# Kernel tuning notes

Hardware: AMD Instinct MI355X
Metric: run time of the kernel (lower is better)

Reference implementation:

```python
import jax, jax.numpy as jnp
import numpy as np

DIM, H, HD = 512, 8, 64
N_BANK = 4096
EPS = 1e-5


def layernorm(x, g, b):
    m = jnp.mean(x, axis=-1, keepdims=True)
    v = jnp.mean(jnp.square(x - m), axis=-1, keepdims=True)
    return (x - m) * jax.lax.rsqrt(v + EPS) * g + b


def setup_inputs() -> dict:
    key = jax.random.key(0)
    ks = jax.random.split(key, 8)
    # xavier_uniform bound for square (512,512) linears
    bound = float(np.sqrt(6.0 / (DIM + DIM)))
    inp = {
        "x_q": jax.random.normal(ks[0], (32, 128, DIM), jnp.float32),
        "x_k": jax.random.normal(ks[1], (N_BANK, DIM), jnp.float32),
        "x_v": jax.random.normal(ks[2], (N_BANK, DIM), jnp.float32),
        "Wq": jax.random.uniform(ks[3], (DIM, DIM), jnp.float32, -bound, bound),
        "Wk": jax.random.uniform(ks[4], (DIM, DIM), jnp.float32, -bound, bound),
        "Wv": jax.random.uniform(ks[5], (DIM, DIM), jnp.float32, -bound, bound),
        "Wproj": jax.random.uniform(ks[6], (DIM, DIM), jnp.float32, -bound, bound),
        "qn_g": jnp.ones((HD,), jnp.float32),
        "qn_b": jnp.zeros((HD,), jnp.float32),
        "kn_g": jnp.ones((HD,), jnp.float32),
        "kn_b": jnp.zeros((HD,), jnp.float32),
        "n_g": jnp.ones((DIM,), jnp.float32),
        "n_b": jnp.zeros((DIM,), jnp.float32),
    }
    return inp


def reference(x_q, x_k, x_v, Wq, Wk, Wv, Wproj, qn_g, qn_b, kn_g, kn_b, n_g, n_b):
    B, S, D = x_q.shape
    N = x_k.shape[0]
    scale = HD ** (-0.5)
    # Linear layers (torch: y = x @ W.T)
    q = jnp.einsum('bsd,od->bso', x_q, Wq).reshape(B, S, H, HD).transpose(0, 2, 1, 3)  # (B,H,S,hd)
    k = jnp.einsum('nd,od->no', x_k, Wk).reshape(N, H, HD).transpose(1, 0, 2)          # (H,N,hd)
    v = jnp.einsum('nd,od->no', x_v, Wv).reshape(N, H, HD).transpose(1, 0, 2)          # (H,N,hd)
    # per-head qk layernorm
    q = layernorm(q, qn_g, qn_b) * scale
    k = layernorm(k, kn_g, kn_b)
    # cross-attention to shared bank (K/V have no batch dim)
    attn = jnp.einsum('bhsd,hnd->bhsn', q, k)          # (B,H,S,N)
    attn = jax.nn.softmax(attn, axis=-1)
    x = jnp.einsum('bhsn,hnd->bhsd', attn, v)          # (B,H,S,hd)
    x = x.transpose(0, 2, 1, 3).reshape(B, S, D)
    x = layernorm(x, n_g, n_b)
    x = jnp.einsum('bsd,od->bso', x, Wproj)
    return x
```

## Files before the change

kernel.cpp:

```cpp
#include <hip/hip_runtime.h>
#include <hip/hip_bf16.h>
#include <math.h>

#define DIM 512
#define NHEAD 8
#define HD 64
#define NBANK 4096
#define NQROWS 4096
#define EPS 1e-5f
#define QSCALE 0.125f
#define PART_ELEMS (NQROWS * DIM)

typedef __attribute__((ext_vector_type(4))) float floatx4;
typedef __attribute__((ext_vector_type(8))) short short8;

__device__ __forceinline__ unsigned short f2bf(float f) {
    unsigned int u = __float_as_uint(f);
    u += 0x7fffu + ((u >> 16) & 1u);
    return (unsigned short)(u >> 16);
}
__device__ __forceinline__ float bf2f(unsigned short h) {
    return __uint_as_float(((unsigned int)h) << 16);
}
__device__ __forceinline__ unsigned int pk2(float a, float b) {
    union { __hip_bfloat162 h; unsigned int u; } cvt;
    cvt.h = __float22bfloat162_rn(make_float2(a, b));
    return cvt.u;
}

__global__ __launch_bounds__(256) void wcvt_kernel(
    const float* __restrict__ Wq, const float* __restrict__ Wk,
    const float* __restrict__ Wv, const float* __restrict__ Wp,
    unsigned short* __restrict__ Wb)
{
    const float* src = (blockIdx.y == 0) ? Wq : (blockIdx.y == 1) ? Wk
                     : (blockIdx.y == 2) ? Wv : Wp;
    unsigned short* dst = Wb + (size_t)blockIdx.y * DIM * DIM;
    const int i = (blockIdx.x * 256 + threadIdx.x) * 8;
    const float4 a0 = *(const float4*)(src + i);
    const float4 a1 = *(const float4*)(src + i + 4);
    union { short8 v; unsigned int u[4]; } t;
    t.u[0] = pk2(a0.x, a0.y); t.u[1] = pk2(a0.z, a0.w);
    t.u[2] = pk2(a1.x, a1.y); t.u[3] = pk2(a1.z, a1.w);
    *(short8*)(dst + i) = t.v;
}

__global__ __launch_bounds__(256) void qkv_kernel(
    const float* __restrict__ xq, const float* __restrict__ xk, const float* __restrict__ xv,
    const unsigned short* __restrict__ Wb,
    const float* __restrict__ qg, const float* __restrict__ qbeta,
    const float* __restrict__ kg, const float* __restrict__ kbeta,
    unsigned short* __restrict__ Qb, unsigned short* __restrict__ Kb,
    unsigned short* __restrict__ VTb)
{
    __shared__ short8 smem[3072];
    const int tid  = threadIdx.x;
    const int w    = tid >> 6, lane = tid & 63, m = lane & 15, q = lane >> 4;
    const int wr   = w & 1, wc = w >> 1;
    const int row0 = blockIdx.x * 64;
    const int mat  = blockIdx.y >> 2;
    const int col0 = (blockIdx.y & 3) * 128;
    const float* X = (mat == 0) ? xq : (mat == 1) ? xk : xv;
    const unsigned short* Wm = Wb + (size_t)mat * DIM * DIM;

    const int arow0 = tid >> 3,           aseg = tid & 7;
    const int arow1 = (tid + 256) >> 3;
    const float* ap0 = X + (size_t)(row0 + arow0) * DIM + aseg * 8;
    const float* ap1 = X + (size_t)(row0 + arow1) * DIM + aseg * 8;
    const int adst0 = arow0 * 8 + (aseg ^ (arow0 & 7));
    const int adst1 = arow1 * 8 + (aseg ^ (arow1 & 7));
    int brow[4], bdst[4];
    const unsigned short* bp[4];
    #pragma unroll
    for (int j = 0; j < 4; ++j) {
        const int idx = tid + j * 256;
        brow[j] = idx >> 3; const int seg = idx & 7;
        bp[j] = Wm + (size_t)(col0 + brow[j]) * DIM + seg * 8;
        bdst[j] = brow[j] * 8 + (seg ^ (brow[j] & 7));
    }

    floatx4 acc[2][4];
    #pragma unroll
    for (int mt = 0; mt < 2; ++mt)
        #pragma unroll
        for (int nt = 0; nt < 4; ++nt) acc[mt][nt] = (floatx4){0.f, 0.f, 0.f, 0.f};

    float4 pa[4];
    short8 pb[4];

    pa[0] = *(const float4*)(ap0);     pa[1] = *(const float4*)(ap0 + 4);
    pa[2] = *(const float4*)(ap1);     pa[3] = *(const float4*)(ap1 + 4);
    #pragma unroll
    for (int j = 0; j < 4; ++j) pb[j] = *(const short8*)(bp[j]);
    {
        short8* as = smem; short8* bs = smem + 512;
        union { short8 v; unsigned int u[4]; } ta;
        ta.u[0] = pk2(pa[0].x, pa[0].y); ta.u[1] = pk2(pa[0].z, pa[0].w);
        ta.u[2] = pk2(pa[1].x, pa[1].y); ta.u[3] = pk2(pa[1].z, pa[1].w);
        as[adst0] = ta.v;
        ta.u[0] = pk2(pa[2].x, pa[2].y); ta.u[1] = pk2(pa[2].z, pa[2].w);
        ta.u[2] = pk2(pa[3].x, pa[3].y); ta.u[3] = pk2(pa[3].z, pa[3].w);
        as[adst1] = ta.v;
        #pragma unroll
        for (int j = 0; j < 4; ++j) bs[bdst[j]] = pb[j];
    }
    pa[0] = *(const float4*)(ap0 + 64);  pa[1] = *(const float4*)(ap0 + 68);
    pa[2] = *(const float4*)(ap1 + 64);  pa[3] = *(const float4*)(ap1 + 68);
    #pragma unroll
    for (int j = 0; j < 4; ++j) pb[j] = *(const short8*)(bp[j] + 64);
    __syncthreads();

    for (int kt = 0; kt < 8; ++kt) {
        short8* as  = smem + (kt & 1) * 1536;
        short8* bs  = as + 512;
        short8* asn = smem + ((kt + 1) & 1) * 1536;
        short8* bsn = asn + 512;
        if (kt < 7) {
            union { short8 v; unsigned int u[4]; } ta;
            ta.u[0] = pk2(pa[0].x, pa[0].y); ta.u[1] = pk2(pa[0].z, pa[0].w);
            ta.u[2] = pk2(pa[1].x, pa[1].y); ta.u[3] = pk2(pa[1].z, pa[1].w);
            asn[adst0] = ta.v;
            ta.u[0] = pk2(pa[2].x, pa[2].y); ta.u[1] = pk2(pa[2].z, pa[2].w);
            ta.u[2] = pk2(pa[3].x, pa[3].y); ta.u[3] = pk2(pa[3].z, pa[3].w);
            asn[adst1] = ta.v;
            #pragma unroll
            for (int j = 0; j < 4; ++j) bsn[bdst[j]] = pb[j];
        }
        if (kt < 6) {
            const int o = (kt + 2) * 64;
            pa[0] = *(const float4*)(ap0 + o);  pa[1] = *(const float4*)(ap0 + o + 4);
            pa[2] = *(const float4*)(ap1 + o);  pa[3] = *(const float4*)(ap1 + o + 4);
            #pragma unroll
            for (int j = 0; j < 4; ++j) pb[j] = *(const short8*)(bp[j] + o);
        }
        #pragma unroll
        for (int s = 0; s < 2; ++s) {
            short8 af[2], bfr[4];
            #pragma unroll
            for (int mt = 0; mt < 2; ++mt)
                af[mt] = as[(wr * 32 + mt * 16 + m) * 8 + ((s * 4 + q) ^ (m & 7))];
            #pragma unroll
            for (int nt = 0; nt < 4; ++nt)
                bfr[nt] = bs[(wc * 64 + nt * 16 + m) * 8 + ((s * 4 + q) ^ (m & 7))];
            #pragma unroll
            for (int mt = 0; mt < 2; ++mt)
                #pragma unroll
                for (int nt = 0; nt < 4; ++nt)
                    acc[mt][nt] = __builtin_amdgcn_mfma_f32_16x16x32_bf16(af[mt], bfr[nt], acc[mt][nt], 0, 0, 0);
        }
        __syncthreads();
    }

    if (mat < 2) {
        const float* g = (mat == 0) ? qg : kg;
        const float* be = (mat == 0) ? qbeta : kbeta;
        unsigned short* Y = (mat == 0) ? Qb : Kb;
        float gv[4], bv[4];
        #pragma unroll
        for (int nt = 0; nt < 4; ++nt) { gv[nt] = g[nt * 16 + m]; bv[nt] = be[nt * 16 + m]; }
        #pragma unroll
        for (int mt = 0; mt < 2; ++mt) {
            #pragma unroll
            for (int r = 0; r < 4; ++r) {
                float s = 0.f, sq = 0.f;
                #pragma unroll
                for (int nt = 0; nt < 4; ++nt) { const float v = acc[mt][nt][r]; s += v; sq += v * v; }
                s  += __shfl_xor(s, 1);  s  += __shfl_xor(s, 2);  s  += __shfl_xor(s, 4);  s  += __shfl_xor(s, 8);
                sq += __shfl_xor(sq, 1); sq += __shfl_xor(sq, 2); sq += __shfl_xor(sq, 4); sq += __shfl_xor(sq, 8);
                const float mean = s * (1.f / HD);
                const float var  = sq * (1.f / HD) - mean * mean;
                const float rr   = rsqrtf(var + EPS);
                const int grow = row0 + wr * 32 + mt * 16 + q * 4 + r;
                #pragma unroll
                for (int nt = 0; nt < 4; ++nt) {
                    float v = (acc[mt][nt][r] - mean) * rr * gv[nt] + bv[nt];
                    if (mat == 0) v *= QSCALE;
                    Y[(size_t)grow * DIM + col0 + wc * 64 + nt * 16 + m] = f2bf(v);
                }
            }
        }
    } else {
        unsigned short* vt = (unsigned short*)smem;
        #pragma unroll
        for (int mt = 0; mt < 2; ++mt)
            #pragma unroll
            for (int nt = 0; nt < 4; ++nt) {
                const int c  = wc * 64 + nt * 16 + m;
                const int rw = wr * 32 + mt * 16 + q * 4;
                *(unsigned int*)(vt + c * 88 + rw)     = pk2(acc[mt][nt][0], acc[mt][nt][1]);
                *(unsigned int*)(vt + c * 88 + rw + 2) = pk2(acc[mt][nt][2], acc[mt][nt][3]);
            }
        __syncthreads();
        #pragma unroll
        for (int p = 0; p < 4; ++p) {
            const int idx = tid + p * 256;
            const int c = idx >> 3, sg = idx & 7;
            *(short8*)(VTb + (size_t)(col0 + c) * NBANK + row0 + sg * 8) =
                *(const short8*)(vt + c * 88 + sg * 8);
        }
    }
}

__global__ __launch_bounds__(256) void attn_kernel(
    const unsigned short* __restrict__ Qb, const unsigned short* __restrict__ Kb,
    const unsigned short* __restrict__ VTb, unsigned short* __restrict__ AOp,
    float* __restrict__ sums)
{
    __shared__ short8 smem[2048];
    const int tid  = threadIdx.x;
    const int w    = tid >> 6;
    const int lane = tid & 63;
    const int m    = lane & 15;
    const int Qd   = lane >> 4;
    const int h    = blockIdx.x & 7;
    const int qgi  = blockIdx.x >> 3;
    const int row0 = qgi * 128;
    const int part = blockIdx.y;
    const int base0 = part * 1024;

    const int sn0 = tid >> 3,        sseg = tid & 7;
    const int sn1 = (tid + 256) >> 3;
    const int kd0 = sn0 * 8 + (sseg ^ (sn0 & 7));
    const int kd1 = sn1 * 8 + (sseg ^ (sn1 & 7));
    const unsigned short* kp0 = Kb + (size_t)sn0 * DIM + h * HD + sseg * 8;
    const unsigned short* kp1 = Kb + (size_t)sn1 * DIM + h * HD + sseg * 8;
    const unsigned short* vp0 = VTb + (size_t)(h * HD + sn0) * NBANK + (sseg >> 2) * 32 + (sseg & 3) * 4;
    const unsigned short* vp1 = VTb + (size_t)(h * HD + sn1) * NBANK + (sseg >> 2) * 32 + (sseg & 3) * 4;

    short8 qf[2][2];
    #pragma unroll
    for (int mt = 0; mt < 2; ++mt)
        #pragma unroll
        for (int s = 0; s < 2; ++s)
            qf[mt][s] = *(const short8*)(Qb + (size_t)(row0 + w * 32 + mt * 16 + m) * DIM
                                         + h * HD + s * 32 + Qd * 8);

    floatx4 of[4][2];
    float sump[2] = {0.f, 0.f};
    #pragma unroll
    for (int t = 0; t < 4; ++t)
        #pragma unroll
        for (int mt = 0; mt < 2; ++mt) of[t][mt] = (floatx4){0.f, 0.f, 0.f, 0.f};

    short8 kreg0, kreg1;
    ushort4 vlo0, vhi0, vlo1, vhi1;

    kreg0 = *(const short8*)(kp0 + (size_t)base0 * DIM);
    kreg1 = *(const short8*)(kp1 + (size_t)base0 * DIM);
    vlo0 = *(const ushort4*)(vp0 + base0);  vhi0 = *(const ushort4*)(vp0 + base0 + 16);
    vlo1 = *(const ushort4*)(vp1 + base0);  vhi1 = *(const ushort4*)(vp1 + base0 + 16);
    {
        short8* ks = smem; short8* vts = smem + 512;
        ks[kd0] = kreg0; ks[kd1] = kreg1;
        union { short8 v; ushort4 h4[2]; } tv;
        tv.h4[0] = vlo0; tv.h4[1] = vhi0;  vts[kd0] = tv.v;
        tv.h4[0] = vlo1; tv.h4[1] = vhi1;  vts[kd1] = tv.v;
    }
    kreg0 = *(const short8*)(kp0 + (size_t)(base0 + 64) * DIM);
    kreg1 = *(const short8*)(kp1 + (size_t)(base0 + 64) * DIM);
    vlo0 = *(const ushort4*)(vp0 + base0 + 64);  vhi0 = *(const ushort4*)(vp0 + base0 + 80);
    vlo1 = *(const ushort4*)(vp1 + base0 + 64);  vhi1 = *(const ushort4*)(vp1 + base0 + 80);
    __syncthreads();

    for (int c = 0; c < 16; ++c) {
        short8* ks   = smem + (c & 1) * 1024;
        short8* vts  = ks + 512;
        short8* ksn  = smem + ((c + 1) & 1) * 1024;
        short8* vtsn = ksn + 512;
        if (c < 15) {
            ksn[kd0] = kreg0; ksn[kd1] = kreg1;
            union { short8 v; ushort4 h4[2]; } tv;
            tv.h4[0] = vlo0; tv.h4[1] = vhi0;  vtsn[kd0] = tv.v;
            tv.h4[0] = vlo1; tv.h4[1] = vhi1;  vtsn[kd1] = tv.v;
        }
        if (c < 14) {
            const int nb = base0 + (c + 2) * 64;
            kreg0 = *(const short8*)(kp0 + (size_t)nb * DIM);
            kreg1 = *(const short8*)(kp1 + (size_t)nb * DIM);
            vlo0 = *(const ushort4*)(vp0 + nb);  vhi0 = *(const ushort4*)(vp0 + nb + 16);
            vlo1 = *(const ushort4*)(vp1 + nb);  vhi1 = *(const ushort4*)(vp1 + nb + 16);
        }

        floatx4 st[4][2];
        #pragma unroll
        for (int t = 0; t < 4; ++t)
            #pragma unroll
            for (int mt = 0; mt < 2; ++mt) st[t][mt] = (floatx4){0.f, 0.f, 0.f, 0.f};
        #pragma unroll
        for (int s = 0; s < 2; ++s)
            #pragma unroll
            for (int t = 0; t < 4; ++t) {
                const short8 kf = ks[(t * 16 + m) * 8 + ((s * 4 + Qd) ^ (m & 7))];
                #pragma unroll
                for (int mt = 0; mt < 2; ++mt)
                    st[t][mt] = __builtin_amdgcn_mfma_f32_16x16x32_bf16(kf, qf[mt][s], st[t][mt], 0, 0, 0);
            }

        float p[4][2][4];
        #pragma unroll
        for (int t = 0; t < 4; ++t)
            #pragma unroll
            for (int mt = 0; mt < 2; ++mt)
                #pragma unroll
                for (int r = 0; r < 4; ++r) {
                    const float e = __expf(st[t][mt][r]);
                    p[t][mt][r] = e;
                    sump[mt] += e;
                }
        union { short8 v; unsigned int u[4]; } pf[2][2];
        #pragma unroll
        for (int mt = 0; mt < 2; ++mt)
            #pragma unroll
            for (int s2 = 0; s2 < 2; ++s2)
                #pragma unroll
                for (int u = 0; u < 4; ++u)
                    pf[mt][s2].u[u] = pk2(p[s2 * 2 + (u >> 1)][mt][(u & 1) * 2],
                                          p[s2 * 2 + (u >> 1)][mt][(u & 1) * 2 + 1]);

        #pragma unroll
        for (int s2 = 0; s2 < 2; ++s2)
            #pragma unroll
            for (int t2 = 0; t2 < 4; ++t2) {
                const short8 vf = vts[(t2 * 16 + m) * 8 + ((s2 * 4 + Qd) ^ (m & 7))];
                #pragma unroll
                for (int mt = 0; mt < 2; ++mt)
                    of[t2][mt] = __builtin_amdgcn_mfma_f32_16x16x32_bf16(vf, pf[mt][s2].v, of[t2][mt], 0, 0, 0);
            }
        __syncthreads();
    }

    #pragma unroll
    for (int mt = 0; mt < 2; ++mt) {
        float s = sump[mt];
        s += __shfl_xor(s, 16);
        s += __shfl_xor(s, 32);
        sump[mt] = s;
    }
    if (Qd == 0) {
        #pragma unroll
        for (int mt = 0; mt < 2; ++mt)
            sums[((size_t)part * NQROWS + row0 + w * 32 + mt * 16 + m) * NHEAD + h] = sump[mt];
    }

    unsigned int* ob = (unsigned int*)smem;
    #pragma unroll
    for (int t2 = 0; t2 < 4; ++t2)
        #pragma unroll
        for (int mt = 0; mt < 2; ++mt) {
            const int q  = w * 32 + mt * 16 + m;
            const int blk = t2 * 2 + (Qd >> 1);
            const int sub = (Qd & 1) * 2;
            const int bs  = (blk ^ (q & 7)) * 4;
            ob[q * 32 + bs + sub]     = pk2(of[t2][mt][0], of[t2][mt][1]);
            ob[q * 32 + bs + sub + 1] = pk2(of[t2][mt][2], of[t2][mt][3]);
        }
    __syncthreads();
    #pragma unroll
    for (int pp = 0; pp < 4; ++pp) {
        const int idx = tid + pp * 256;
        const int q = idx >> 3, sg = idx & 7;
        *(short8*)(AOp + (size_t)part * PART_ELEMS + (size_t)(row0 + q) * DIM + h * HD + sg * 8) =
            smem[q * 8 + (sg ^ (q & 7))];
    }
}

__global__ __launch_bounds__(256) void combine_kernel(
    const unsigned short* __restrict__ AOp, const float* __restrict__ sums,
    const float* __restrict__ g, const float* __restrict__ be,
    unsigned short* __restrict__ AO)
{
    __shared__ float rs[256], rq[256], sm[2], sr[2];
    const int tid  = threadIdx.x;
    const int half = tid >> 7;
    const int row  = blockIdx.x * 2 + half;
    const int t    = tid & 127;
    const int h    = t >> 4;

    float stot = 0.f;
    #pragma unroll
    for (int p = 0; p < 4; ++p)
        stot += sums[((size_t)p * NQROWS + row) * NHEAD + h];

    float o[4] = {0.f, 0.f, 0.f, 0.f};
    #pragma unroll
    for (int p = 0; p < 4; ++p) {
        const ushort4 u = *(const ushort4*)(AOp + (size_t)p * PART_ELEMS + (size_t)row * DIM + t * 4);
        o[0] += bf2f(u.x); o[1] += bf2f(u.y); o[2] += bf2f(u.z); o[3] += bf2f(u.w);
    }
    const float inv = 1.0f / stot;
    const float v0 = o[0] * inv, v1 = o[1] * inv, v2 = o[2] * inv, v3 = o[3] * inv;

    rs[tid] = v0 + v1 + v2 + v3;
    rq[tid] = v0 * v0 + v1 * v1 + v2 * v2 + v3 * v3;
    __syncthreads();
    #pragma unroll
    for (int off = 64; off > 0; off >>= 1) {
        if (t < off) { rs[tid] += rs[tid + off]; rq[tid] += rq[tid + off]; }
        __syncthreads();
    }
    if (t == 0) {
        const float mean = rs[tid] * (1.f / DIM);
        const float var  = rq[tid] * (1.f / DIM) - mean * mean;
        sm[half] = mean;
        sr[half] = rsqrtf(var + EPS);
    }
    __syncthreads();

    const float mean = sm[half], rstd = sr[half];
    const float4 g4 = *(const float4*)(g + t * 4);
    const float4 b4 = *(const float4*)(be + t * 4);
    uint2 packed;
    packed.x = pk2((v0 - mean) * rstd * g4.x + b4.x, (v1 - mean) * rstd * g4.y + b4.y);
    packed.y = pk2((v2 - mean) * rstd * g4.z + b4.z, (v3 - mean) * rstd * g4.w + b4.w);
    *(uint2*)(AO + (size_t)row * DIM + t * 4) = packed;
}

__global__ __launch_bounds__(256) void final_kernel(
    const unsigned short* __restrict__ AO, const unsigned short* __restrict__ Wpb,
    float* __restrict__ out)
{
    __shared__ short8 fs[2048];
    const int tid  = threadIdx.x;
    const int w    = tid >> 6, lane = tid & 63, m = lane & 15, q = lane >> 4;
    const int row0 = blockIdx.x * 64;
    const int col0 = blockIdx.y * 64;

    const int r0 = tid >> 3,           sseg = tid & 7;
    const int r1 = (tid + 256) >> 3;
    const int d0 = r0 * 8 + (sseg ^ (r0 & 7));
    const int d1 = r1 * 8 + (sseg ^ (r1 & 7));
    const unsigned short* ap0 = AO  + (size_t)(row0 + r0) * DIM + sseg * 8;
    const unsigned short* ap1 = AO  + (size_t)(row0 + r1) * DIM + sseg * 8;
    const unsigned short* wp0 = Wpb + (size_t)(col0 + r0) * DIM + sseg * 8;
    const unsigned short* wp1 = Wpb + (size_t)(col0 + r1) * DIM + sseg * 8;

    floatx4 acc[4];
    #pragma unroll
    for (int mt = 0; mt < 4; ++mt) acc[mt] = (floatx4){0.f, 0.f, 0.f, 0.f};

    short8 pa0, pa1, pw0, pw1;
    pa0 = *(const short8*)(ap0);       pa1 = *(const short8*)(ap1);
    pw0 = *(const short8*)(wp0);       pw1 = *(const short8*)(wp1);
    {
        fs[d0] = pa0; fs[d1] = pa1;
        fs[512 + d0] = pw0; fs[512 + d1] = pw1;
    }
    pa0 = *(const short8*)(ap0 + 64);  pa1 = *(const short8*)(ap1 + 64);
    pw0 = *(const short8*)(wp0 + 64);  pw1 = *(const short8*)(wp1 + 64);
    __syncthreads();

    for (int kt = 0; kt < 8; ++kt) {
        short8* buf  = fs + (kt & 1) * 1024;
        short8* bufn = fs + ((kt + 1) & 1) * 1024;
        if (kt < 7) {
            bufn[d0] = pa0; bufn[d1] = pa1;
            bufn[512 + d0] = pw0; bufn[512 + d1] = pw1;
        }
        if (kt < 6) {
            const int o = (kt + 2) * 64;
            pa0 = *(const short8*)(ap0 + o);  pa1 = *(const short8*)(ap1 + o);
            pw0 = *(const short8*)(wp0 + o);  pw1 = *(const short8*)(wp1 + o);
        }
        #pragma unroll
        for (int s = 0; s < 2; ++s) {
            short8 af[4];
            #pragma unroll
            for (int mt = 0; mt < 4; ++mt)
                af[mt] = buf[(mt * 16 + m) * 8 + ((s * 4 + q) ^ (m & 7))];
            const short8 bfr = buf[512 + (w * 16 + m) * 8 + ((s * 4 + q) ^ (m & 7))];
            #pragma unroll
            for (int mt = 0; mt < 4; ++mt)
                acc[mt] = __builtin_amdgcn_mfma_f32_16x16x32_bf16(af[mt], bfr, acc[mt], 0, 0, 0);
        }
        __syncthreads();
    }

    #pragma unroll
    for (int mt = 0; mt < 4; ++mt)
        #pragma unroll
        for (int r = 0; r < 4; ++r)
            out[(size_t)(row0 + mt * 16 + q * 4 + r) * DIM + col0 + w * 16 + m] = acc[mt][r];
}

extern "C" void kernel_launch(void* const* d_in, const int* in_sizes, int n_in,
                              void* d_out, int out_size, void* d_ws, size_t ws_size,
                              hipStream_t stream)
{
    const float* x_q = (const float*)d_in[0];
    const float* x_k = (const float*)d_in[1];
    const float* x_v = (const float*)d_in[2];
    const float* Wq  = (const float*)d_in[3];
    const float* Wk  = (const float*)d_in[4];
    const float* Wv  = (const float*)d_in[5];
    const float* Wp  = (const float*)d_in[6];
    const float* qg  = (const float*)d_in[7];
    const float* qb  = (const float*)d_in[8];
    const float* kg  = (const float*)d_in[9];
    const float* kb  = (const float*)d_in[10];
    const float* ng  = (const float*)d_in[11];
    const float* nb  = (const float*)d_in[12];
    float* out = (float*)d_out;

    unsigned short* Qb   = (unsigned short*)d_ws;
    unsigned short* Kb   = Qb  + (size_t)NQROWS * DIM;
    unsigned short* VTb  = Kb  + (size_t)NBANK * DIM;
    unsigned short* AOp  = VTb + (size_t)NBANK * DIM;
    float*          sums = (float*)(AOp + (size_t)4 * PART_ELEMS);
    unsigned short* Wb   = (unsigned short*)(sums + (size_t)4 * NQROWS * NHEAD);
    unsigned short* AO   = Qb;

    wcvt_kernel<<<dim3(128, 4), 256, 0, stream>>>(Wq, Wk, Wv, Wp, Wb);
    qkv_kernel<<<dim3(64, 12), 256, 0, stream>>>(x_q, x_k, x_v, Wb,
                                                 qg, qb, kg, kb, Qb, Kb, VTb);
    attn_kernel<<<dim3(256, 4), 256, 0, stream>>>(Qb, Kb, VTb, AOp, sums);
    combine_kernel<<<NQROWS / 2, 256, 0, stream>>>(AOp, sums, ng, nb, AO);
    final_kernel<<<dim3(64, 8), 256, 0, stream>>>(AO, Wb + (size_t)3 * DIM * DIM, out);
}
```

Measured before the change: 171.5 us.

## Load GEMM and attention tiles straight into LDS via global_load_lds with pre-swizzled layouts

Replaces the register-staged global loads and LDS stores for the bf16 operands (weights, K, V-transpose, attention output) with direct global-to-LDS transfers. Because these transfers cannot apply the XOR swizzle on the way in, the producers now write their outputs in global memory already swizzled and tiled: the weight conversion, the K projection epilogue, the V-transpose writer and the layernorm output. This cuts register pressure and VALU/LDS-store instructions in the inner loops. The cost is coupled layout changes across several kernels and a dependence on the async LDS transfers being complete at the existing barriers.

```diff
diff --git a/kernel.cpp b/kernel.cpp
--- a/kernel.cpp
+++ b/kernel.cpp
@@ -26,6 +26,11 @@
     union { __hip_bfloat162 h; unsigned int u; } cvt;
     cvt.h = __float22bfloat162_rn(make_float2(a, b));
     return cvt.u;
+}
+__device__ __forceinline__ void dma16(const void* gsrc, void* ldst) {
+    __builtin_amdgcn_global_load_lds(
+        (const __attribute__((address_space(1))) unsigned int*)gsrc,
+        (__attribute__((address_space(3))) unsigned int*)ldst, 16, 0, 0);
 }
 
 __global__ __launch_bounds__(256) void wcvt_kernel(
@@ -37,12 +42,14 @@
                      : (blockIdx.y == 2) ? Wv : Wp;
     unsigned short* dst = Wb + (size_t)blockIdx.y * DIM * DIM;
     const int i = (blockIdx.x * 256 + threadIdx.x) * 8;
+    const int row = i >> 9, kpos = i & 511;
+    const int kt = kpos >> 6, seg = (kpos >> 3) & 7;
     const float4 a0 = *(const float4*)(src + i);
     const float4 a1 = *(const float4*)(src + i + 4);
     union { short8 v; unsigned int u[4]; } t;
     t.u[0] = pk2(a0.x, a0.y); t.u[1] = pk2(a0.z, a0.w);
     t.u[2] = pk2(a1.x, a1.y); t.u[3] = pk2(a1.z, a1.w);
-    *(short8*)(dst + i) = t.v;
+    *(short8*)(dst + (size_t)row * 512 + kt * 64 + ((seg ^ (row & 7)) << 3)) = t.v;
 }
 
 __global__ __launch_bounds__(256) void qkv_kernel(
@@ -69,14 +76,11 @@
     const float* ap1 = X + (size_t)(row0 + arow1) * DIM + aseg * 8;
     const int adst0 = arow0 * 8 + (aseg ^ (arow0 & 7));
     const int adst1 = arow1 * 8 + (aseg ^ (arow1 & 7));
-    int brow[4], bdst[4];
-    const unsigned short* bp[4];
+    const unsigned short* bsrc[4];
     #pragma unroll
     for (int j = 0; j < 4; ++j) {
-        const int idx = tid + j * 256;
-        brow[j] = idx >> 3; const int seg = idx & 7;
-        bp[j] = Wm + (size_t)(col0 + brow[j]) * DIM + seg * 8;
-        bdst[j] = brow[j] * 8 + (seg ^ (brow[j] & 7));
+        const int item = j * 256 + tid;
+        bsrc[j] = Wm + (size_t)(col0 + (item >> 3)) * DIM + (item & 7) * 8;
     }
 
     floatx4 acc[2][4];
@@ -86,12 +90,8 @@
         for (int nt = 0; nt < 4; ++nt) acc[mt][nt] = (floatx4){0.f, 0.f, 0.f, 0.f};
 
     float4 pa[4];
-    short8 pb[4];
-
     pa[0] = *(const float4*)(ap0);     pa[1] = *(const float4*)(ap0 + 4);
     pa[2] = *(const float4*)(ap1);     pa[3] = *(const float4*)(ap1 + 4);
-    #pragma unroll
-    for (int j = 0; j < 4; ++j) pb[j] = *(const short8*)(bp[j]);
     {
         short8* as = smem; short8* bs = smem + 512;
         union { short8 v; unsigned int u[4]; } ta;
@@ -102,12 +102,11 @@
         ta.u[2] = pk2(pa[3].x, pa[3].y); ta.u[3] = pk2(pa[3].z, pa[3].w);
         as[adst1] = ta.v;
         #pragma unroll
-        for (int j = 0; j < 4; ++j) bs[bdst[j]] = pb[j];
+        for (int j = 0; j < 4; ++j)
+            dma16(bsrc[j], bs + j * 256 + w * 64);
     }
     pa[0] = *(const float4*)(ap0 + 64);  pa[1] = *(const float4*)(ap0 + 68);
     pa[2] = *(const float4*)(ap1 + 64);  pa[3] = *(const float4*)(ap1 + 68);
-    #pragma unroll
-    for (int j = 0; j < 4; ++j) pb[j] = *(const short8*)(bp[j] + 64);
     __syncthreads();
 
     for (int kt = 0; kt < 8; ++kt) {
@@ -124,14 +123,13 @@
             ta.u[2] = pk2(pa[3].x, pa[3].y); ta.u[3] = pk2(pa[3].z, pa[3].w);
             asn[adst1] = ta.v;
             #pragma unroll
-            for (int j = 0; j < 4; ++j) bsn[bdst[j]] = pb[j];
+            for (int j = 0; j < 4; ++j)
+                dma16(bsrc[j] + (kt + 1) * 64, bsn + j * 256 + w * 64);
         }
         if (kt < 6) {
             const int o = (kt + 2) * 64;
             pa[0] = *(const float4*)(ap0 + o);  pa[1] = *(const float4*)(ap0 + o + 4);
             pa[2] = *(const float4*)(ap1 + o);  pa[3] = *(const float4*)(ap1 + o + 4);
-            #pragma unroll
-            for (int j = 0; j < 4; ++j) pb[j] = *(const short8*)(bp[j] + o);
         }
         #pragma unroll
         for (int s = 0; s < 2; ++s) {
@@ -175,12 +173,19 @@
                 for (int nt = 0; nt < 4; ++nt) {
                     float v = (acc[mt][nt][r] - mean) * rr * gv[nt] + bv[nt];
                     if (mat == 0) v *= QSCALE;
-                    Y[(size_t)grow * DIM + col0 + wc * 64 + nt * 16 + m] = f2bf(v);
+                    const int col = col0 + wc * 64 + nt * 16 + m;
+                    int scol = col;
+                    if (mat == 1) {
+                        const int o = col & 63, sg2 = o >> 3;
+                        scol = (col & ~63) | (((sg2 ^ (grow & 7)) << 3) | (o & 7));
+                    }
+                    Y[(size_t)grow * DIM + scol] = f2bf(v);
                 }
             }
         }
     } else {
         unsigned short* vt = (unsigned short*)smem;
+        __syncthreads();
         #pragma unroll
         for (int mt = 0; mt < 2; ++mt)
             #pragma unroll
@@ -193,10 +198,15 @@
         __syncthreads();
         #pragma unroll
         for (int p = 0; p < 4; ++p) {
-            const int idx = tid + p * 256;
-            const int c = idx >> 3, sg = idx & 7;
-            *(short8*)(VTb + (size_t)(col0 + c) * NBANK + row0 + sg * 8) =
-                *(const short8*)(vt + c * 88 + sg * 8);
+            const int idx = p * 256 + tid;
+            const int c = idx >> 3, g = idx & 7;
+            const int dglob = col0 + c, hh = dglob >> 6, dl = dglob & 63;
+            const int pos = (g >> 2) * 32 + (g & 3) * 4;
+            union { short8 v; ushort4 h4[2]; } tv;
+            tv.h4[0] = *(const ushort4*)(vt + c * 88 + pos);
+            tv.h4[1] = *(const ushort4*)(vt + c * 88 + pos + 16);
+            *(short8*)(VTb + ((size_t)(hh * 64 + blockIdx.x) * 512
+                              + dl * 8 + (g ^ (dl & 7))) * 8) = tv.v;
         }
     }
 }
@@ -216,16 +226,12 @@
     const int qgi  = blockIdx.x >> 3;
     const int row0 = qgi * 128;
     const int part = blockIdx.y;
-    const int base0 = part * 1024;
-
-    const int sn0 = tid >> 3,        sseg = tid & 7;
-    const int sn1 = (tid + 256) >> 3;
-    const int kd0 = sn0 * 8 + (sseg ^ (sn0 & 7));
-    const int kd1 = sn1 * 8 + (sseg ^ (sn1 & 7));
-    const unsigned short* kp0 = Kb + (size_t)sn0 * DIM + h * HD + sseg * 8;
-    const unsigned short* kp1 = Kb + (size_t)sn1 * DIM + h * HD + sseg * 8;
-    const unsigned short* vp0 = VTb + (size_t)(h * HD + sn0) * NBANK + (sseg >> 2) * 32 + (sseg & 3) * 4;
-    const unsigned short* vp1 = VTb + (size_t)(h * HD + sn1) * NBANK + (sseg >> 2) * 32 + (sseg & 3) * 4;
+    const int c0   = part * 16;
+
+    const int it0 = tid, it1 = tid + 256;
+    const unsigned short* ksrc0 = Kb + (size_t)(it0 >> 3) * DIM + h * HD + (it0 & 7) * 8;
+    const unsigned short* ksrc1 = Kb + (size_t)(it1 >> 3) * DIM + h * HD + (it1 & 7) * 8;
+    const unsigned short* vbase = VTb + (size_t)h * 64 * 512 * 8;
 
     short8 qf[2][2];
     #pragma unroll
@@ -242,43 +248,26 @@
         #pragma unroll
         for (int mt = 0; mt < 2; ++mt) of[t][mt] = (floatx4){0.f, 0.f, 0.f, 0.f};
 
-    short8 kreg0, kreg1;
-    ushort4 vlo0, vhi0, vlo1, vhi1;
-
-    kreg0 = *(const short8*)(kp0 + (size_t)base0 * DIM);
-    kreg1 = *(const short8*)(kp1 + (size_t)base0 * DIM);
-    vlo0 = *(const ushort4*)(vp0 + base0);  vhi0 = *(const ushort4*)(vp0 + base0 + 16);
-    vlo1 = *(const ushort4*)(vp1 + base0);  vhi1 = *(const ushort4*)(vp1 + base0 + 16);
     {
         short8* ks = smem; short8* vts = smem + 512;
-        ks[kd0] = kreg0; ks[kd1] = kreg1;
-        union { short8 v; ushort4 h4[2]; } tv;
-        tv.h4[0] = vlo0; tv.h4[1] = vhi0;  vts[kd0] = tv.v;
-        tv.h4[0] = vlo1; tv.h4[1] = vhi1;  vts[kd1] = tv.v;
-    }
-    kreg0 = *(const short8*)(kp0 + (size_t)(base0 + 64) * DIM);
-    kreg1 = *(const short8*)(kp1 + (size_t)(base0 + 64) * DIM);
-    vlo0 = *(const ushort4*)(vp0 + base0 + 64);  vhi0 = *(const ushort4*)(vp0 + base0 + 80);
-    vlo1 = *(const ushort4*)(vp1 + base0 + 64);  vhi1 = *(const ushort4*)(vp1 + base0 + 80);
+        dma16(ksrc0 + (size_t)c0 * 64 * DIM, ks + w * 64);
+        dma16(ksrc1 + (size_t)c0 * 64 * DIM, ks + 256 + w * 64);
+        dma16(vbase + ((size_t)c0 * 512 + it0) * 8, vts + w * 64);
+        dma16(vbase + ((size_t)c0 * 512 + it1) * 8, vts + 256 + w * 64);
+    }
     __syncthreads();
 
     for (int c = 0; c < 16; ++c) {
-        short8* ks   = smem + (c & 1) * 1024;
-        short8* vts  = ks + 512;
-        short8* ksn  = smem + ((c + 1) & 1) * 1024;
-        short8* vtsn = ksn + 512;
+        short8* ks  = smem + (c & 1) * 1024;
+        short8* vts = ks + 512;
         if (c < 15) {
-            ksn[kd0] = kreg0; ksn[kd1] = kreg1;
-            union { short8 v; ushort4 h4[2]; } tv;
-            tv.h4[0] = vlo0; tv.h4[1] = vhi0;  vtsn[kd0] = tv.v;
-            tv.h4[0] = vlo1; tv.h4[1] = vhi1;  vtsn[kd1] = tv.v;
-        }
-        if (c < 14) {
-            const int nb = base0 + (c + 2) * 64;
-            kreg0 = *(const short8*)(kp0 + (size_t)nb * DIM);
-            kreg1 = *(const short8*)(kp1 + (size_t)nb * DIM);
-            vlo0 = *(const ushort4*)(vp0 + nb);  vhi0 = *(const ushort4*)(vp0 + nb + 16);
-            vlo1 = *(const ushort4*)(vp1 + nb);  vhi1 = *(const ushort4*)(vp1 + nb + 16);
+            short8* ksn  = smem + ((c + 1) & 1) * 1024;
+            short8* vtsn = ksn + 512;
+            const size_t nc = c0 + c + 1;
+            dma16(ksrc0 + nc * 64 * DIM, ksn + w * 64);
+            dma16(ksrc1 + nc * 64 * DIM, ksn + 256 + w * 64);
+            dma16(vbase + (nc * 512 + it0) * 8, vtsn + w * 64);
+            dma16(vbase + (nc * 512 + it1) * 8, vtsn + 256 + w * 64);
         }
 
         floatx4 st[4][2];
@@ -347,20 +336,20 @@
     for (int t2 = 0; t2 < 4; ++t2)
         #pragma unroll
         for (int mt = 0; mt < 2; ++mt) {
-            const int q  = w * 32 + mt * 16 + m;
+            const int qq  = w * 32 + mt * 16 + m;
             const int blk = t2 * 2 + (Qd >> 1);
             const int sub = (Qd & 1) * 2;
-            const int bs  = (blk ^ (q & 7)) * 4;
-            ob[q * 32 + bs + sub]     = pk2(of[t2][mt][0], of[t2][mt][1]);
-            ob[q * 32 + bs + sub + 1] = pk2(of[t2][mt][2], of[t2][mt][3]);
+            const int bs  = (blk ^ (qq & 7)) * 4;
+            ob[qq * 32 + bs + sub]     = pk2(of[t2][mt][0], of[t2][mt][1]);
+            ob[qq * 32 + bs + sub + 1] = pk2(of[t2][mt][2], of[t2][mt][3]);
         }
     __syncthreads();
     #pragma unroll
     for (int pp = 0; pp < 4; ++pp) {
         const int idx = tid + pp * 256;
-        const int q = idx >> 3, sg = idx & 7;
-        *(short8*)(AOp + (size_t)part * PART_ELEMS + (size_t)(row0 + q) * DIM + h * HD + sg * 8) =
-            smem[q * 8 + (sg ^ (q & 7))];
+        const int qq = idx >> 3, sg = idx & 7;
+        *(short8*)(AOp + (size_t)part * PART_ELEMS + (size_t)(row0 + qq) * DIM + h * HD + sg * 8) =
+            smem[qq * 8 + (sg ^ (qq & 7))];
     }
 }
 
@@ -412,7 +401,8 @@
     uint2 packed;
     packed.x = pk2((v0 - mean) * rstd * g4.x + b4.x, (v1 - mean) * rstd * g4.y + b4.y);
     packed.y = pk2((v2 - mean) * rstd * g4.z + b4.z, (v3 - mean) * rstd * g4.w + b4.w);
-    *(uint2*)(AO + (size_t)row * DIM + t * 4) = packed;
+    const int kt = t >> 4, seg = (t >> 1) & 7, jof = (t & 1) * 4;
+    *(uint2*)(AO + (size_t)row * DIM + kt * 64 + ((seg ^ (row & 7)) << 3) + jof) = packed;
 }
 
 __global__ __launch_bounds__(256) void final_kernel(
@@ -425,41 +415,33 @@
     const int row0 = blockIdx.x * 64;
     const int col0 = blockIdx.y * 64;
 
-    const int r0 = tid >> 3,           sseg = tid & 7;
-    const int r1 = (tid + 256) >> 3;
-    const int d0 = r0 * 8 + (sseg ^ (r0 & 7));
-    const int d1 = r1 * 8 + (sseg ^ (r1 & 7));
-    const unsigned short* ap0 = AO  + (size_t)(row0 + r0) * DIM + sseg * 8;
-    const unsigned short* ap1 = AO  + (size_t)(row0 + r1) * DIM + sseg * 8;
-    const unsigned short* wp0 = Wpb + (size_t)(col0 + r0) * DIM + sseg * 8;
-    const unsigned short* wp1 = Wpb + (size_t)(col0 + r1) * DIM + sseg * 8;
+    const int it0 = tid, it1 = tid + 256;
+    const unsigned short* asrc0 = AO  + (size_t)(row0 + (it0 >> 3)) * DIM + (it0 & 7) * 8;
+    const unsigned short* asrc1 = AO  + (size_t)(row0 + (it1 >> 3)) * DIM + (it1 & 7) * 8;
+    const unsigned short* wsrc0 = Wpb + (size_t)(col0 + (it0 >> 3)) * DIM + (it0 & 7) * 8;
+    const unsigned short* wsrc1 = Wpb + (size_t)(col0 + (it1 >> 3)) * DIM + (it1 & 7) * 8;
 
     floatx4 acc[4];
     #pragma unroll
     for (int mt = 0; mt < 4; ++mt) acc[mt] = (floatx4){0.f, 0.f, 0.f, 0.f};
 
-    short8 pa0, pa1, pw0, pw1;
-    pa0 = *(const short8*)(ap0);       pa1 = *(const short8*)(ap1);
-    pw0 = *(const short8*)(wp0);       pw1 = *(const short8*)(wp1);
     {
-        fs[d0] = pa0; fs[d1] = pa1;
-        fs[512 + d0] = pw0; fs[512 + d1] = pw1;
-    }
-    pa0 = *(const short8*)(ap0 + 64);  pa1 = *(const short8*)(ap1 + 64);
-    pw0 = *(const short8*)(wp0 + 64);  pw1 = *(const short8*)(wp1 + 64);
+        dma16(asrc0, fs + w * 64);
+        dma16(asrc1, fs + 256 + w * 64);
+        dma16(wsrc0, fs + 512 + w * 64);
+        dma16(wsrc1, fs + 768 + w * 64);
+    }
     __syncthreads();
 
     for (int kt = 0; kt < 8; ++kt) {
         short8* buf  = fs + (kt & 1) * 1024;
-        short8* bufn = fs + ((kt + 1) & 1) * 1024;
         if (kt < 7) {
-            bufn[d0] = pa0; bufn[d1] = pa1;
-            bufn[512 + d0] = pw0; bufn[512 + d1] = pw1;
-        }
-        if (kt < 6) {
-            const int o = (kt + 2) * 64;
-            pa0 = *(const short8*)(ap0 + o);  pa1 = *(const short8*)(ap1 + o);
-            pw0 = *(const short8*)(wp0 + o);  pw1 = *(const short8*)(wp1 + o);
+            short8* bufn = fs + ((kt + 1) & 1) * 1024;
+            const int o = (kt + 1) * 64;
+            dma16(asrc0 + o, bufn + w * 64);
+            dma16(asrc1 + o, bufn + 256 + w * 64);
+            dma16(wsrc0 + o, bufn + 512 + w * 64);
+            dma16(wsrc1 + o, bufn + 768 + w * 64);
         }
         #pragma unroll
         for (int s = 0; s < 2; ++s) {
```

New measurement: 170.2 us. Within noise of the previous version (-0.7%).
